# Optimization experiments

Measured on AMD Instinct MI355X. Metric: run time of the kernel, lower is better.

## Reference

```python
import jax, jax.numpy as jnp
import numpy as np

H, W = 14, 14
HEAD_DIM = 32
HEADS = 24
HIDDEN = 768
RATE = 0.2
EPS = 1e-5


def _bias_idxs(h, w):
    # map_bias indexing: for flat pair index x over (h*w)^2
    x = jnp.arange(h * h * w * w)
    m, n = x // (h * w), x % (h * w)
    i, j = m // w, m % w
    ip, jp = n // w, n % w
    return (i - ip + h) * (2 * w) + (j - jp + w)


def _layer_norm(x, g, b):
    mu = jnp.mean(x, axis=-1, keepdims=True)
    var = jnp.mean(jnp.square(x - mu), axis=-1, keepdims=True)
    return (x - mu) * jax.lax.rsqrt(var + EPS) * g + b


def setup_inputs() -> dict:
    key = jax.random.key(0)
    ks = jax.random.split(key, 10)
    N, L = 64, H * W
    s = lambda fan_in: 1.0 / np.sqrt(fan_in)
    return {
        "x": jax.random.normal(ks[0], (N, L, HIDDEN), jnp.float32),
        "rel_bias": jax.random.uniform(ks[1], (1, 2 * H * 2 * W), jnp.float32, -0.5, 0.5),
        "wq": jax.random.normal(ks[2], (HEAD_DIM, HEAD_DIM), jnp.float32) * s(HEAD_DIM),
        "wk": jax.random.normal(ks[3], (HEAD_DIM, HEAD_DIM), jnp.float32) * s(HEAD_DIM),
        "wv": jax.random.normal(ks[4], (HEAD_DIM, HEAD_DIM), jnp.float32) * s(HEAD_DIM),
        "w_out": jax.random.normal(ks[5], (HIDDEN, HIDDEN), jnp.float32) * s(HIDDEN),
        "ln1_g": jnp.ones((HIDDEN,), jnp.float32),
        "ln1_b": jnp.zeros((HIDDEN,), jnp.float32),
        "ln2_g": jnp.ones((HIDDEN,), jnp.float32),
        "ln2_b": jnp.zeros((HIDDEN,), jnp.float32),
        "w1": jax.random.normal(ks[6], (4 * HIDDEN, HIDDEN), jnp.float32) * s(HIDDEN),
        "b1": jnp.zeros((4 * HIDDEN,), jnp.float32),
        "w2": jax.random.normal(ks[7], (HIDDEN, 4 * HIDDEN), jnp.float32) * s(4 * HIDDEN),
        "b2": jnp.zeros((HIDDEN,), jnp.float32),
    }


def reference(x, rel_bias, wq, wk, wv, w_out, ln1_g, ln1_b, ln2_g, ln2_b, w1, b1, w2, b2):
    N, L, _ = x.shape

    def attn(m):
        xh = m.reshape(N, L, HEADS, HEAD_DIM)
        # Linear(head_dim, head_dim) shared across heads; torch Linear: y = x @ W^T
        q = jnp.einsum("nlhd,ed->nlhe", xh, wq)
        k = jnp.einsum("nlhd,ed->nlhe", xh, wk)
        v = jnp.einsum("nlhd,ed->nlhe", xh, wv)
        scores = jnp.einsum("nqhd,nkhd->nhqk", q, k)
        bias = rel_bias[0][_bias_idxs(H, W)].reshape(1, 1, L, L)
        a = jax.nn.softmax((scores + bias) / np.sqrt(HEAD_DIM), axis=-1)
        o = jnp.einsum("nhqk,nkhd->nqhd", a, v).reshape(N, L, HIDDEN)
        return o @ w_out.T

    def ffn(m):
        h = jax.nn.gelu(m @ w1.T + b1, approximate=False)
        return h @ w2.T + b2

    # training-mode stochastic depth: deterministic scaling by RATE
    x = (x + attn(_layer_norm(x, ln1_g, ln1_b))) * RATE
    x = (x + ffn(_layer_norm(x, ln2_g, ln2_b))) * RATE
    return x
```

## Files before the change

### kernel.cpp

```cpp
#include <hip/hip_runtime.h>
#include <math.h>

#define NB    64
#define LSEQ  196
#define HID   768
#define NHEAD 24
#define HDIM  32
#define FFN   3072
#define ROWS  (NB * LSEQ)
#define RATE  0.2f
#define LN_EPS 1e-5f

typedef unsigned short bf16_t;
typedef short s16x8 __attribute__((ext_vector_type(8)));
typedef float f32x4 __attribute__((ext_vector_type(4)));

__device__ __forceinline__ unsigned short f2bf(float f) {
    unsigned u = __float_as_uint(f);
    unsigned r = u + 0x7fffu + ((u >> 16) & 1u);
    return (unsigned short)(r >> 16);
}

#define GLOAD_LDS16(g, l)                                                  \
    __builtin_amdgcn_global_load_lds(                                      \
        (const __attribute__((address_space(1))) void*)(g),                \
        (__attribute__((address_space(3))) void*)(l), 16, 0, 0)

#define WOUT4 (HID * HID / 4)
#define W14   (FFN * HID / 4)
__global__ __launch_bounds__(256) void cvt_w_kernel(
    const float* __restrict__ w_out, const float* __restrict__ w1,
    const float* __restrict__ w2, bf16_t* __restrict__ wob,
    bf16_t* __restrict__ w1b, bf16_t* __restrict__ w2b)
{
    int i = blockIdx.x * 256 + threadIdx.x;
    const float* src; bf16_t* dst; int off;
    if (i < WOUT4)            { src = w_out; dst = wob; off = i; }
    else if (i < WOUT4 + W14) { src = w1;    dst = w1b; off = i - WOUT4; }
    else                      { src = w2;    dst = w2b; off = i - WOUT4 - W14; }
    float4 v = ((const float4*)src)[off];
    uint2 p;
    p.x = (unsigned)f2bf(v.x) | ((unsigned)f2bf(v.y) << 16);
    p.y = (unsigned)f2bf(v.z) | ((unsigned)f2bf(v.w) << 16);
    ((uint2*)dst)[off] = p;
}

__global__ __launch_bounds__(256) void ln_kernel(
    const float* __restrict__ x, const float* __restrict__ g,
    const float* __restrict__ b, bf16_t* __restrict__ yv)
{
    int row = blockIdx.x;
    int tid = threadIdx.x;
    const float* xr = x + (size_t)row * HID;
    float v0 = xr[tid], v1 = xr[tid + 256], v2 = xr[tid + 512];
    __shared__ float rs[256], rs2[256];
    rs[tid]  = v0 + v1 + v2;
    rs2[tid] = v0 * v0 + v1 * v1 + v2 * v2;
    __syncthreads();
    for (int off = 128; off > 0; off >>= 1) {
        if (tid < off) { rs[tid] += rs[tid + off]; rs2[tid] += rs2[tid + off]; }
        __syncthreads();
    }
    float mean = rs[0] * (1.0f / HID);
    float var  = rs2[0] * (1.0f / HID) - mean * mean;
    float rstd = rsqrtf(var + LN_EPS);
    bf16_t* yr = yv + (size_t)row * HID;
    yr[tid]       = f2bf((v0 - mean) * rstd * g[tid]       + b[tid]);
    yr[tid + 256] = f2bf((v1 - mean) * rstd * g[tid + 256] + b[tid + 256]);
    yr[tid + 512] = f2bf((v2 - mean) * rstd * g[tid + 512] + b[tid + 512]);
}

#define QKV_T 16
__global__ __launch_bounds__(256) void ln_qkv_mfma_kernel(
    const float* __restrict__ x, const float* __restrict__ g,
    const float* __restrict__ b,
    const float* __restrict__ wq, const float* __restrict__ wk,
    const float* __restrict__ wv,
    bf16_t* __restrict__ q, bf16_t* __restrict__ k, bf16_t* __restrict__ v)
{
    int tid = threadIdx.x;
    int w = tid >> 6, lane = tid & 63;
    int lr = lane & 15, lq = lane >> 4;

    __shared__ __align__(16) bf16_t Xs[QKV_T * 24 * 32];
    __shared__ __align__(16) bf16_t Wqs[32 * 32];
    __shared__ __align__(16) bf16_t Wks[32 * 32];
    __shared__ __align__(16) bf16_t Wvs[32 * 32];

    for (int i = tid; i < 1024; i += 256) {
        Wqs[i] = f2bf(wq[i]);
        Wks[i] = f2bf(wk[i]);
        Wvs[i] = f2bf(wv[i]);
    }

    float4 gv[3], bv[3];
#pragma unroll
    for (int i = 0; i < 3; i++) {
        gv[i] = ((const float4*)g)[lane + i * 64];
        bv[i] = ((const float4*)b)[lane + i * 64];
    }

    for (int j = 0; j < 4; j++) {
        int lt = w * 4 + j;
        size_t row = (size_t)blockIdx.x * QKV_T + lt;
        const float4* xr = (const float4*)(x + row * HID);
        float4 xv[3];
        float s = 0.f, s2 = 0.f;
#pragma unroll
        for (int i = 0; i < 3; i++) {
            xv[i] = xr[lane + i * 64];
            s  += xv[i].x + xv[i].y + xv[i].z + xv[i].w;
            s2 += xv[i].x * xv[i].x + xv[i].y * xv[i].y
                + xv[i].z * xv[i].z + xv[i].w * xv[i].w;
        }
#pragma unroll
        for (int d = 1; d < 64; d <<= 1) {
            s  += __shfl_xor(s, d);
            s2 += __shfl_xor(s2, d);
        }
        float mean = s * (1.0f / HID);
        float rstd = rsqrtf(s2 * (1.0f / HID) - mean * mean + LN_EPS);
#pragma unroll
        for (int i = 0; i < 3; i++) {
            int idx  = (lane + i * 64) * 4;
            int head = idx >> 5, d0 = idx & 31;
            float o0 = (xv[i].x - mean) * rstd * gv[i].x + bv[i].x;
            float o1 = (xv[i].y - mean) * rstd * gv[i].y + bv[i].y;
            float o2 = (xv[i].z - mean) * rstd * gv[i].z + bv[i].z;
            float o3 = (xv[i].w - mean) * rstd * gv[i].w + bv[i].w;
            uint2 p;
            p.x = (unsigned)f2bf(o0) | ((unsigned)f2bf(o1) << 16);
            p.y = (unsigned)f2bf(o2) | ((unsigned)f2bf(o3) << 16);
            *(uint2*)&Xs[(lt * 24 + head) * 32 + d0] = p;
        }
    }
    __syncthreads();

    s16x8 bq[2], bk[2], bvv[2];
    bq[0]  = *(const s16x8*)&Wqs[lr * 32 + lq * 8];
    bq[1]  = *(const s16x8*)&Wqs[(16 + lr) * 32 + lq * 8];
    bk[0]  = *(const s16x8*)&Wks[lr * 32 + lq * 8];
    bk[1]  = *(const s16x8*)&Wks[(16 + lr) * 32 + lq * 8];
    bvv[0] = *(const s16x8*)&Wvs[lr * 32 + lq * 8];
    bvv[1] = *(const s16x8*)&Wvs[(16 + lr) * 32 + lq * 8];

    for (int t = 0; t < 6; t++) {
        int tile = w * 6 + t;
        s16x8 aX = *(const s16x8*)&Xs[(tile * 16 + lr) * 32 + lq * 8];
        f32x4 z = {};
        f32x4 aq0 = __builtin_amdgcn_mfma_f32_16x16x32_bf16(aX, bq[0],  z, 0, 0, 0);
        f32x4 aq1 = __builtin_amdgcn_mfma_f32_16x16x32_bf16(aX, bq[1],  z, 0, 0, 0);
        f32x4 ak0 = __builtin_amdgcn_mfma_f32_16x16x32_bf16(aX, bk[0],  z, 0, 0, 0);
        f32x4 ak1 = __builtin_amdgcn_mfma_f32_16x16x32_bf16(aX, bk[1],  z, 0, 0, 0);
        f32x4 av0 = __builtin_amdgcn_mfma_f32_16x16x32_bf16(aX, bvv[0], z, 0, 0, 0);
        f32x4 av1 = __builtin_amdgcn_mfma_f32_16x16x32_bf16(aX, bvv[1], z, 0, 0, 0);
        int rbase = tile * 16 + lq * 4;
#pragma unroll
        for (int r = 0; r < 4; r++) {
            int xrow = rbase + r;
            int t_loc = xrow / 24, head = xrow - t_loc * 24;
            size_t gb = ((size_t)blockIdx.x * QKV_T + t_loc) * HID + head * 32;
            q[gb + lr]      = f2bf(aq0[r]);
            q[gb + 16 + lr] = f2bf(aq1[r]);
            k[gb + lr]      = f2bf(ak0[r]);
            k[gb + 16 + lr] = f2bf(ak1[r]);
            v[gb + lr]      = f2bf(av0[r]);
            v[gb + 16 + lr] = f2bf(av1[r]);
        }
    }
}

#define VT_S 232
#define P_S  40

__global__ __launch_bounds__(256) void attn_mfma_kernel(
    const bf16_t* __restrict__ q, const bf16_t* __restrict__ k,
    const bf16_t* __restrict__ v, const float* __restrict__ rel_bias,
    bf16_t* __restrict__ o)
{
    int h = blockIdx.x;
    int n = blockIdx.y;
    int tid = threadIdx.x;
    int w = tid >> 6, lane = tid & 63;
    int lr = lane & 15;
    int lq = lane >> 4;

    __shared__ __align__(16) bf16_t Qs[208 * 32];
    __shared__ __align__(16) bf16_t Ks[224 * 32];
    __shared__ __align__(16) bf16_t Vt[32 * VT_S];
    __shared__ float bsh[28 * 28];
    __shared__ __align__(16) bf16_t Ps[4][16 * P_S];

    size_t base = (size_t)n * LSEQ * HID + (size_t)h * HDIM;

    for (int i = tid; i < 224 * 4; i += 256) {
        int r = i >> 2, c = i & 3;
        uint4 kv = make_uint4(0, 0, 0, 0);
        if (r < 196) kv = *(const uint4*)&k[base + (size_t)r * HID + c * 8];
        *(uint4*)&Ks[r * 32 + c * 8] = kv;
        if (r < 208) {
            uint4 qv = make_uint4(0, 0, 0, 0);
            if (r < 196) qv = *(const uint4*)&q[base + (size_t)r * HID + c * 8];
            *(uint4*)&Qs[r * 32 + c * 8] = qv;
        }
    }
    for (int i = tid; i < 196 * 16; i += 256) {
        int key = i >> 4, d2 = (i & 15) * 2;
        unsigned u = *(const unsigned*)&v[base + (size_t)key * HID + d2];
        Vt[d2 * VT_S + key]       = (bf16_t)(u & 0xffffu);
        Vt[(d2 + 1) * VT_S + key] = (bf16_t)(u >> 16);
    }
    for (int i = tid; i < 32 * 32; i += 256) {
        int d = i >> 5, kp = i & 31;
        if (kp < 28) Vt[d * VT_S + 196 + kp] = 0;
    }
    for (int i = tid; i < 784; i += 256) bsh[i] = rel_bias[i];
    __syncthreads();

    const float inv_sqrt_d = 0.17677669529663687f;
    bf16_t* P = Ps[w];

    for (int qt = w; qt < 13; qt += 4) {
        s16x8 aQ = *(const s16x8*)&Qs[(qt * 16 + lr) * 32 + lq * 8];

        int bb[4]; bool qvalid[4];
#pragma unroll
        for (int r = 0; r < 4; r++) {
            int qr = qt * 16 + lq * 4 + r;
            qvalid[r] = qr < LSEQ;
            int qq = qvalid[r] ? qr : 0;
            int qi = qq / 14, qj = qq - 14 * (qq / 14);
            bb[r] = (qi + 14) * 28 + (qj + 14);
        }

        f32x4 sf[14];
#pragma unroll
        for (int kt = 0; kt < 14; kt++) {
            s16x8 bK = *(const s16x8*)&Ks[(kt * 16 + lr) * 32 + lq * 8];
            f32x4 z = {};
            sf[kt] = __builtin_amdgcn_mfma_f32_16x16x32_bf16(aQ, bK, z, 0, 0, 0);
        }
#pragma unroll
        for (int kt = 0; kt < 14; kt++) {
            int key = kt * 16 + lr;
            bool kv = key < LSEQ;
            int kk2 = kv ? key : 0;
            int ip = kk2 / 14, jp = kk2 - 14 * ip;
            int boff = ip * 28 + jp;
#pragma unroll
            for (int r = 0; r < 4; r++) {
                float val = (sf[kt][r] + bsh[bb[r] - boff]) * inv_sqrt_d;
                sf[kt][r] = kv ? val : -1e30f;
            }
        }
        float mx[4];
#pragma unroll
        for (int r = 0; r < 4; r++) {
            float m = sf[0][r];
#pragma unroll
            for (int kt = 1; kt < 14; kt++) m = fmaxf(m, sf[kt][r]);
            mx[r] = m;
        }
#pragma unroll
        for (int d = 1; d < 16; d <<= 1)
#pragma unroll
            for (int r = 0; r < 4; r++)
                mx[r] = fmaxf(mx[r], __shfl_xor(mx[r], d));
        float sum[4] = {0.f, 0.f, 0.f, 0.f};
#pragma unroll
        for (int kt = 0; kt < 14; kt++)
#pragma unroll
            for (int r = 0; r < 4; r++) {
                float p = __expf(sf[kt][r] - mx[r]);
                sf[kt][r] = p;
                sum[r] += p;
            }
#pragma unroll
        for (int d = 1; d < 16; d <<= 1)
#pragma unroll
            for (int r = 0; r < 4; r++)
                sum[r] += __shfl_xor(sum[r], d);

        f32x4 oacc[2] = {};
#pragma unroll
        for (int kc = 0; kc < 7; kc++) {
#pragma unroll
            for (int r = 0; r < 4; r++) {
                P[(lq * 4 + r) * P_S + lr]      = f2bf(sf[2 * kc][r]);
                P[(lq * 4 + r) * P_S + 16 + lr] = f2bf(sf[2 * kc + 1][r]);
            }
            s16x8 aP = *(const s16x8*)&P[lr * P_S + lq * 8];
#pragma unroll
            for (int dt = 0; dt < 2; dt++) {
                s16x8 bV = *(const s16x8*)&Vt[(dt * 16 + lr) * VT_S + kc * 32 + lq * 8];
                oacc[dt] = __builtin_amdgcn_mfma_f32_16x16x32_bf16(aP, bV, oacc[dt], 0, 0, 0);
            }
        }
#pragma unroll
        for (int r = 0; r < 4; r++) {
            if (qvalid[r]) {
                float inv_l = 1.0f / sum[r];
                size_t ob = base + (size_t)(qt * 16 + lq * 4 + r) * HID;
                o[ob + lr]      = f2bf(oacc[0][r] * inv_l);
                o[ob + 16 + lr] = f2bf(oacc[1][r] * inv_l);
            }
        }
    }
}

__device__ __forceinline__ float gelu_fast(float x) {
    float z2 = 1.5957691216f * (x + 0.044715f * x * x * x);
    return x - x * __frcp_rn(__expf(z2) + 1.0f);
}

template <int MODE, bool OBF, int TM>
__global__ __launch_bounds__(256) void gemm_mfma(
    const bf16_t* __restrict__ A, const bf16_t* __restrict__ B,
    void* __restrict__ Cv, int M, int N, int K,
    const float* __restrict__ bias, const float* __restrict__ res, float scale)
{
    constexpr int MT = TM / 32;
    __shared__ __align__(16) bf16_t As[TM * 64];
    __shared__ __align__(16) bf16_t Bs[128 * 64];

    int tid = threadIdx.x;
    int mb = M / TM, nb = N >> 7;
    int gblk = blockIdx.x;
    int full = mb & ~7;
    int gfull = full * nb;
    int m_, n_;
    if (gblk < gfull) {
        int sg = gblk / (8 * nb), u = gblk - sg * (8 * nb);
        m_ = sg * 8 + (u & 7); n_ = u >> 3;
    } else {
        int u = gblk - gfull, rem = mb - full;
        m_ = full + u % rem; n_ = u / rem;
    }
    int bm = m_ * TM, bn = n_ << 7;

    int w    = tid >> 6;
    int lane = tid & 63;
    int wm = (w & 1) * (TM / 2);
    int wn = (w >> 1) * 64;
    int lr = lane & 15;
    int lq = lane >> 4;

    int srowl = lane >> 3;
    int scb   = ((lane & 7) ^ srowl) * 16;
    const char* Ab = (const char*)A;
    const char* Bb = (const char*)B;

    f32x4 acc[MT][4] = {};

    for (int k0 = 0; k0 < K; k0 += 64) {
#pragma unroll
        for (int j = 0; j < TM / 32; j++) {
            int rb = w * (TM / 4) + j * 8;
            GLOAD_LDS16(Ab + ((size_t)(bm + rb + srowl) * K + k0) * 2 + scb, &As[rb * 64]);
        }
#pragma unroll
        for (int j = 0; j < 4; j++) {
            int rb = w * 32 + j * 8;
            GLOAD_LDS16(Bb + ((size_t)(bn + rb + srowl) * K + k0) * 2 + scb, &Bs[rb * 64]);
        }
        __syncthreads();

        int sw = lr & 7;
#pragma unroll
        for (int kc = 0; kc < 2; kc++) {
            int cof = (((kc << 2) | lq) ^ sw) * 8;
            s16x8 af[MT], bf[4];
#pragma unroll
            for (int t = 0; t < MT; t++)
                af[t] = *(const s16x8*)&As[(wm + t * 16 + lr) * 64 + cof];
#pragma unroll
            for (int t = 0; t < 4; t++)
                bf[t] = *(const s16x8*)&Bs[(wn + t * 16 + lr) * 64 + cof];
#pragma unroll
            for (int tm = 0; tm < MT; tm++)
#pragma unroll
                for (int tn = 0; tn < 4; tn++)
                    acc[tm][tn] = __builtin_amdgcn_mfma_f32_16x16x32_bf16(
                        af[tm], bf[tn], acc[tm][tn], 0, 0, 0);
        }
        __syncthreads();
    }

#pragma unroll
    for (int tm = 0; tm < MT; tm++) {
#pragma unroll
        for (int tn = 0; tn < 4; tn++) {
#pragma unroll
            for (int r = 0; r < 4; r++) {
                int mrow = bm + wm + tm * 16 + lq * 4 + r;
                int ncol = bn + wn + tn * 16 + lr;
                float vacc = acc[tm][tn][r];
                if (MODE == 1) {
                    vacc = (res[(size_t)mrow * N + ncol] + vacc) * scale;
                } else if (MODE == 2) {
                    vacc = gelu_fast(vacc + bias[ncol]);
                } else if (MODE == 3) {
                    vacc = (res[(size_t)mrow * N + ncol] + vacc + bias[ncol]) * scale;
                }
                if (OBF) ((bf16_t*)Cv)[(size_t)mrow * N + ncol] = f2bf(vacc);
                else     ((float*)Cv)[(size_t)mrow * N + ncol] = vacc;
            }
        }
    }
}

template <int MODE, bool OBF>
__global__ __launch_bounds__(512, 2) void gemm_pipe(
    const bf16_t* __restrict__ A, const bf16_t* __restrict__ B,
    void* __restrict__ Cv, int M, int N, int K,
    const float* __restrict__ bias, const float* __restrict__ res, float scale)
{
    constexpr int BM = 256, BN = 128, BK = 64, NBUF = 3;
    __shared__ __align__(16) bf16_t As[NBUF][BM * BK];
    __shared__ __align__(16) bf16_t Bs[NBUF][BN * BK];

    int tid  = threadIdx.x;
    int w    = tid >> 6;
    int lane = tid & 63;

    int mb = M / BM, nb = N / BN;
    int gblk = blockIdx.x;
    int full = mb & ~7;
    int gfull = full * nb;
    int m_, n_;
    if (gblk < gfull) {
        int sg = gblk / (8 * nb), u = gblk - sg * (8 * nb);
        m_ = sg * 8 + (u & 7); n_ = u >> 3;
    } else {
        int u = gblk - gfull, rem = mb - full;
        m_ = full + u % rem; n_ = u / rem;
    }
    int bm = m_ * BM, bn = n_ * BN;

    int wm = (w >> 1) * 64;
    int wn = (w & 1) * 64;
    int lr = lane & 15;
    int lq = lane >> 4;

    int srowl = lane >> 3;
    int scb   = ((lane & 7) ^ srowl) * 16;
    const char* Ab = (const char*)A;
    const char* Bb = (const char*)B;

    const int NT = K / BK;
    f32x4 acc[4][4] = {};

    auto stage = [&](int t, int bi) {
        int k0 = t * BK;
#pragma unroll
        for (int j = 0; j < 4; j++) {
            int rb = j * 64 + w * 8;
            GLOAD_LDS16(Ab + ((size_t)(bm + rb + srowl) * K + k0) * 2 + scb,
                        &As[bi][rb * BK]);
        }
#pragma unroll
        for (int j = 0; j < 2; j++) {
            int rb = j * 64 + w * 8;
            GLOAD_LDS16(Bb + ((size_t)(bn + rb + srowl) * K + k0) * 2 + scb,
                        &Bs[bi][rb * BK]);
        }
    };

    auto compute = [&](int bi) {
        int sw = lr & 7;
        __builtin_amdgcn_s_setprio(1);
#pragma unroll
        for (int kc = 0; kc < 2; kc++) {
            int cof = (((kc << 2) | lq) ^ sw) * 8;
            s16x8 af[4], bf[4];
#pragma unroll
            for (int t = 0; t < 4; t++)
                af[t] = *(const s16x8*)&As[bi][(wm + t * 16 + lr) * BK + cof];
#pragma unroll
            for (int t = 0; t < 4; t++)
                bf[t] = *(const s16x8*)&Bs[bi][(wn + t * 16 + lr) * BK + cof];
#pragma unroll
            for (int tm = 0; tm < 4; tm++)
#pragma unroll
                for (int tn = 0; tn < 4; tn++)
                    acc[tm][tn] = __builtin_amdgcn_mfma_f32_16x16x32_bf16(
                        af[tm], bf[tn], acc[tm][tn], 0, 0, 0);
        }
        __builtin_amdgcn_s_setprio(0);
    };

    stage(0, 0);
    stage(1, 1);

    for (int t = 0; t < NT - 2; t++) {
        stage(t + 2, (t + 2) % 3);
        asm volatile("s_waitcnt vmcnt(12)" ::: "memory");
        __builtin_amdgcn_s_barrier();
        asm volatile("" ::: "memory");
        compute(t % 3);
        asm volatile("" ::: "memory");
        __builtin_amdgcn_s_barrier();
    }
    asm volatile("s_waitcnt vmcnt(6)" ::: "memory");
    __builtin_amdgcn_s_barrier();
    asm volatile("" ::: "memory");
    compute((NT - 2) % 3);
    asm volatile("s_waitcnt vmcnt(0)" ::: "memory");
    __builtin_amdgcn_s_barrier();
    asm volatile("" ::: "memory");
    compute((NT - 1) % 3);

#pragma unroll
    for (int tm = 0; tm < 4; tm++) {
#pragma unroll
        for (int tn = 0; tn < 4; tn++) {
#pragma unroll
            for (int r = 0; r < 4; r++) {
                int mrow = bm + wm + tm * 16 + lq * 4 + r;
                int ncol = bn + wn + tn * 16 + lr;
                float vacc = acc[tm][tn][r];
                if (MODE == 1) {
                    vacc = (res[(size_t)mrow * N + ncol] + vacc) * scale;
                } else if (MODE == 2) {
                    vacc = gelu_fast(vacc + bias[ncol]);
                } else if (MODE == 3) {
                    vacc = (res[(size_t)mrow * N + ncol] + vacc + bias[ncol]) * scale;
                }
                if (OBF) ((bf16_t*)Cv)[(size_t)mrow * N + ncol] = f2bf(vacc);
                else     ((float*)Cv)[(size_t)mrow * N + ncol] = vacc;
            }
        }
    }
}

extern "C" void kernel_launch(void* const* d_in, const int* in_sizes, int n_in,
                              void* d_out, int out_size, void* d_ws, size_t ws_size,
                              hipStream_t stream)
{
    const float* x        = (const float*)d_in[0];
    const float* rel_bias = (const float*)d_in[1];
    const float* wq       = (const float*)d_in[2];
    const float* wk       = (const float*)d_in[3];
    const float* wv       = (const float*)d_in[4];
    const float* w_out    = (const float*)d_in[5];
    const float* ln1_g    = (const float*)d_in[6];
    const float* ln1_b    = (const float*)d_in[7];
    const float* ln2_g    = (const float*)d_in[8];
    const float* ln2_b    = (const float*)d_in[9];
    const float* w1       = (const float*)d_in[10];
    const float* b1       = (const float*)d_in[11];
    const float* w2       = (const float*)d_in[12];
    const float* b2       = (const float*)d_in[13];
    float* out = (float*)d_out;
    float* ws  = (float*)d_ws;

    const size_t SZ = (size_t)ROWS * HID;
    bf16_t* q_bf = (bf16_t*)(ws + SZ);
    bf16_t* k_bf = (bf16_t*)(ws + 2 * SZ);
    bf16_t* v_bf = (bf16_t*)(ws + 3 * SZ);
    bf16_t* o_bf = (bf16_t*)ws;
    bf16_t* y2b  = (bf16_t*)(ws + SZ / 2);
    bf16_t* h    = (bf16_t*)(ws + SZ);
    bf16_t* wob  = (bf16_t*)(ws + 4 * SZ);
    bf16_t* w1b  = wob + (size_t)HID * HID;
    bf16_t* w2b  = w1b + (size_t)FFN * HID;

    cvt_w_kernel<<<(WOUT4 + 2 * W14 + 255) / 256, 256, 0, stream>>>(
        w_out, w1, w2, wob, w1b, w2b);

    ln_qkv_mfma_kernel<<<ROWS / QKV_T, 256, 0, stream>>>(
        x, ln1_g, ln1_b, wq, wk, wv, q_bf, k_bf, v_bf);

    attn_mfma_kernel<<<dim3(NHEAD, NB), 256, 0, stream>>>(q_bf, k_bf, v_bf, rel_bias, o_bf);

    gemm_mfma<1, false, 64><<<(ROWS / 64) * (HID / 128), 256, 0, stream>>>(
        o_bf, wob, out, ROWS, HID, HID, nullptr, x, RATE);

    ln_kernel<<<ROWS, 256, 0, stream>>>(out, ln2_g, ln2_b, y2b);

    gemm_pipe<2, true><<<(ROWS / 256) * (FFN / 128), 512, 0, stream>>>(
        y2b, w1b, h, ROWS, FFN, HID, b1, nullptr, 1.0f);

    gemm_pipe<3, false><<<(ROWS / 256) * (HID / 128), 512, 0, stream>>>(
        h, w2b, out, ROWS, HID, FFN, b2, out, RATE);
}
```

Before: 499.1 us.

## Double-buffer small GEMM and swap FFN GEMMs to wide/single-buffered tiles

Result: faster. 483.4 us (-3.1%).

```diff
diff --git a/kernel.cpp b/kernel.cpp
--- a/kernel.cpp
+++ b/kernel.cpp
@@ -320,8 +320,8 @@
     const float* __restrict__ bias, const float* __restrict__ res, float scale)
 {
     constexpr int MT = TM / 32;
-    __shared__ __align__(16) bf16_t As[TM * 64];
-    __shared__ __align__(16) bf16_t Bs[128 * 64];
+    __shared__ __align__(16) bf16_t As[2][TM * 64];
+    __shared__ __align__(16) bf16_t Bs[2][128 * 64];
 
     int tid = threadIdx.x;
     int mb = M / TM, nb = N >> 7;
@@ -352,19 +352,22 @@
 
     f32x4 acc[MT][4] = {};
 
-    for (int k0 = 0; k0 < K; k0 += 64) {
+    auto stage = [&](int k0, int bi) {
 #pragma unroll
         for (int j = 0; j < TM / 32; j++) {
             int rb = w * (TM / 4) + j * 8;
-            GLOAD_LDS16(Ab + ((size_t)(bm + rb + srowl) * K + k0) * 2 + scb, &As[rb * 64]);
+            GLOAD_LDS16(Ab + ((size_t)(bm + rb + srowl) * K + k0) * 2 + scb,
+                        &As[bi][rb * 64]);
         }
 #pragma unroll
         for (int j = 0; j < 4; j++) {
             int rb = w * 32 + j * 8;
-            GLOAD_LDS16(Bb + ((size_t)(bn + rb + srowl) * K + k0) * 2 + scb, &Bs[rb * 64]);
-        }
-        __syncthreads();
-
+            GLOAD_LDS16(Bb + ((size_t)(bn + rb + srowl) * K + k0) * 2 + scb,
+                        &Bs[bi][rb * 64]);
+        }
+    };
+
+    auto compute = [&](int bi) {
         int sw = lr & 7;
 #pragma unroll
         for (int kc = 0; kc < 2; kc++) {
@@ -372,10 +375,10 @@
             s16x8 af[MT], bf[4];
 #pragma unroll
             for (int t = 0; t < MT; t++)
-                af[t] = *(const s16x8*)&As[(wm + t * 16 + lr) * 64 + cof];
+                af[t] = *(const s16x8*)&As[bi][(wm + t * 16 + lr) * 64 + cof];
 #pragma unroll
             for (int t = 0; t < 4; t++)
-                bf[t] = *(const s16x8*)&Bs[(wn + t * 16 + lr) * 64 + cof];
+                bf[t] = *(const s16x8*)&Bs[bi][(wn + t * 16 + lr) * 64 + cof];
 #pragma unroll
             for (int tm = 0; tm < MT; tm++)
 #pragma unroll
@@ -383,8 +386,22 @@
                     acc[tm][tn] = __builtin_amdgcn_mfma_f32_16x16x32_bf16(
                         af[tm], bf[tn], acc[tm][tn], 0, 0, 0);
         }
-        __syncthreads();
-    }
+    };
+
+    stage(0, 0);
+    asm volatile("s_waitcnt vmcnt(0)" ::: "memory");
+    __builtin_amdgcn_s_barrier();
+
+    const int nt = K >> 6;
+    int cur = 0;
+    for (int t = 0; t < nt - 1; ++t) {
+        stage((t + 1) << 6, cur ^ 1);
+        compute(cur);
+        asm volatile("s_waitcnt vmcnt(0)" ::: "memory");
+        __builtin_amdgcn_s_barrier();
+        cur ^= 1;
+    }
+    compute(cur);
 
 #pragma unroll
     for (int tm = 0; tm < MT; tm++) {
@@ -410,20 +427,16 @@
 }
 
 template <int MODE, bool OBF>
-__global__ __launch_bounds__(512, 2) void gemm_pipe(
+__global__ __launch_bounds__(256) void gemm_wide(
     const bf16_t* __restrict__ A, const bf16_t* __restrict__ B,
     void* __restrict__ Cv, int M, int N, int K,
     const float* __restrict__ bias, const float* __restrict__ res, float scale)
 {
-    constexpr int BM = 256, BN = 128, BK = 64, NBUF = 3;
-    __shared__ __align__(16) bf16_t As[NBUF][BM * BK];
-    __shared__ __align__(16) bf16_t Bs[NBUF][BN * BK];
-
-    int tid  = threadIdx.x;
-    int w    = tid >> 6;
-    int lane = tid & 63;
-
-    int mb = M / BM, nb = N / BN;
+    __shared__ __align__(16) bf16_t As[128 * 64];
+    __shared__ __align__(16) bf16_t Bs[256 * 64];
+
+    int tid = threadIdx.x;
+    int mb = M >> 7, nb = N >> 8;
     int gblk = blockIdx.x;
     int full = mb & ~7;
     int gfull = full * nb;
@@ -435,10 +448,11 @@
         int u = gblk - gfull, rem = mb - full;
         m_ = full + u % rem; n_ = u / rem;
     }
-    int bm = m_ * BM, bn = n_ * BN;
-
-    int wm = (w >> 1) * 64;
-    int wn = (w & 1) * 64;
+    int bm = m_ << 7, bn = n_ << 8;
+
+    int w    = tid >> 6;
+    int lane = tid & 63;
+    int wn = w * 64;
     int lr = lane & 15;
     int lq = lane >> 4;
 
@@ -447,76 +461,51 @@
     const char* Ab = (const char*)A;
     const char* Bb = (const char*)B;
 
-    const int NT = K / BK;
-    f32x4 acc[4][4] = {};
-
-    auto stage = [&](int t, int bi) {
-        int k0 = t * BK;
+    f32x4 acc[8][4] = {};
+
+    for (int k0 = 0; k0 < K; k0 += 64) {
 #pragma unroll
         for (int j = 0; j < 4; j++) {
-            int rb = j * 64 + w * 8;
+            int rb = j * 32 + w * 8;
             GLOAD_LDS16(Ab + ((size_t)(bm + rb + srowl) * K + k0) * 2 + scb,
-                        &As[bi][rb * BK]);
-        }
-#pragma unroll
-        for (int j = 0; j < 2; j++) {
-            int rb = j * 64 + w * 8;
+                        &As[rb * 64]);
+        }
+#pragma unroll
+        for (int j = 0; j < 8; j++) {
+            int rb = j * 32 + w * 8;
             GLOAD_LDS16(Bb + ((size_t)(bn + rb + srowl) * K + k0) * 2 + scb,
-                        &Bs[bi][rb * BK]);
-        }
-    };
-
-    auto compute = [&](int bi) {
+                        &Bs[rb * 64]);
+        }
+        __syncthreads();
+
         int sw = lr & 7;
-        __builtin_amdgcn_s_setprio(1);
 #pragma unroll
         for (int kc = 0; kc < 2; kc++) {
             int cof = (((kc << 2) | lq) ^ sw) * 8;
-            s16x8 af[4], bf[4];
+            s16x8 af[8], bf[4];
+#pragma unroll
+            for (int t = 0; t < 8; t++)
+                af[t] = *(const s16x8*)&As[(t * 16 + lr) * 64 + cof];
 #pragma unroll
             for (int t = 0; t < 4; t++)
-                af[t] = *(const s16x8*)&As[bi][(wm + t * 16 + lr) * BK + cof];
-#pragma unroll
-            for (int t = 0; t < 4; t++)
-                bf[t] = *(const s16x8*)&Bs[bi][(wn + t * 16 + lr) * BK + cof];
-#pragma unroll
-            for (int tm = 0; tm < 4; tm++)
+                bf[t] = *(const s16x8*)&Bs[(wn + t * 16 + lr) * 64 + cof];
+#pragma unroll
+            for (int tm = 0; tm < 8; tm++)
 #pragma unroll
                 for (int tn = 0; tn < 4; tn++)
                     acc[tm][tn] = __builtin_amdgcn_mfma_f32_16x16x32_bf16(
                         af[tm], bf[tn], acc[tm][tn], 0, 0, 0);
         }
-        __builtin_amdgcn_s_setprio(0);
-    };
-
-    stage(0, 0);
-    stage(1, 1);
-
-    for (int t = 0; t < NT - 2; t++) {
-        stage(t + 2, (t + 2) % 3);
-        asm volatile("s_waitcnt vmcnt(12)" ::: "memory");
-        __builtin_amdgcn_s_barrier();
-        asm volatile("" ::: "memory");
-        compute(t % 3);
-        asm volatile("" ::: "memory");
-        __builtin_amdgcn_s_barrier();
-    }
-    asm volatile("s_waitcnt vmcnt(6)" ::: "memory");
-    __builtin_amdgcn_s_barrier();
-    asm volatile("" ::: "memory");
-    compute((NT - 2) % 3);
-    asm volatile("s_waitcnt vmcnt(0)" ::: "memory");
-    __builtin_amdgcn_s_barrier();
-    asm volatile("" ::: "memory");
-    compute((NT - 1) % 3);
-
-#pragma unroll
-    for (int tm = 0; tm < 4; tm++) {
+        __syncthreads();
+    }
+
+#pragma unroll
+    for (int tm = 0; tm < 8; tm++) {
 #pragma unroll
         for (int tn = 0; tn < 4; tn++) {
 #pragma unroll
             for (int r = 0; r < 4; r++) {
-                int mrow = bm + wm + tm * 16 + lq * 4 + r;
+                int mrow = bm + tm * 16 + lq * 4 + r;
                 int ncol = bn + wn + tn * 16 + lr;
                 float vacc = acc[tm][tn][r];
                 if (MODE == 1) {
@@ -578,9 +567,9 @@
 
     ln_kernel<<<ROWS, 256, 0, stream>>>(out, ln2_g, ln2_b, y2b);
 
-    gemm_pipe<2, true><<<(ROWS / 256) * (FFN / 128), 512, 0, stream>>>(
+    gemm_wide<2, true><<<(ROWS / 128) * (FFN / 256), 256, 0, stream>>>(
         y2b, w1b, h, ROWS, FFN, HID, b1, nullptr, 1.0f);
 
-    gemm_pipe<3, false><<<(ROWS / 256) * (HID / 128), 512, 0, stream>>>(
+    gemm_mfma<3, false, 64><<<(ROWS / 64) * (HID / 128), 256, 0, stream>>>(
         h, w2b, out, ROWS, HID, FFN, b2, out, RATE);
 }
```

## Double-buffer small GEMM, split FFN1 pipeline into phases, route FFN2 to small GEMM

Applied to the files above, without the earlier changes.

Measured after the change: 433.8 us. -13.1%, faster.

```diff
diff --git a/kernel.cpp b/kernel.cpp
--- a/kernel.cpp
+++ b/kernel.cpp
@@ -320,8 +320,8 @@
     const float* __restrict__ bias, const float* __restrict__ res, float scale)
 {
     constexpr int MT = TM / 32;
-    __shared__ __align__(16) bf16_t As[TM * 64];
-    __shared__ __align__(16) bf16_t Bs[128 * 64];
+    __shared__ __align__(16) bf16_t As[2][TM * 64];
+    __shared__ __align__(16) bf16_t Bs[2][128 * 64];
 
     int tid = threadIdx.x;
     int mb = M / TM, nb = N >> 7;
@@ -352,19 +352,22 @@
 
     f32x4 acc[MT][4] = {};
 
-    for (int k0 = 0; k0 < K; k0 += 64) {
+    auto stage = [&](int k0, int bi) {
 #pragma unroll
         for (int j = 0; j < TM / 32; j++) {
             int rb = w * (TM / 4) + j * 8;
-            GLOAD_LDS16(Ab + ((size_t)(bm + rb + srowl) * K + k0) * 2 + scb, &As[rb * 64]);
+            GLOAD_LDS16(Ab + ((size_t)(bm + rb + srowl) * K + k0) * 2 + scb,
+                        &As[bi][rb * 64]);
         }
 #pragma unroll
         for (int j = 0; j < 4; j++) {
             int rb = w * 32 + j * 8;
-            GLOAD_LDS16(Bb + ((size_t)(bn + rb + srowl) * K + k0) * 2 + scb, &Bs[rb * 64]);
-        }
-        __syncthreads();
-
+            GLOAD_LDS16(Bb + ((size_t)(bn + rb + srowl) * K + k0) * 2 + scb,
+                        &Bs[bi][rb * 64]);
+        }
+    };
+
+    auto compute = [&](int bi) {
         int sw = lr & 7;
 #pragma unroll
         for (int kc = 0; kc < 2; kc++) {
@@ -372,10 +375,10 @@
             s16x8 af[MT], bf[4];
 #pragma unroll
             for (int t = 0; t < MT; t++)
-                af[t] = *(const s16x8*)&As[(wm + t * 16 + lr) * 64 + cof];
+                af[t] = *(const s16x8*)&As[bi][(wm + t * 16 + lr) * 64 + cof];
 #pragma unroll
             for (int t = 0; t < 4; t++)
-                bf[t] = *(const s16x8*)&Bs[(wn + t * 16 + lr) * 64 + cof];
+                bf[t] = *(const s16x8*)&Bs[bi][(wn + t * 16 + lr) * 64 + cof];
 #pragma unroll
             for (int tm = 0; tm < MT; tm++)
 #pragma unroll
@@ -383,8 +386,22 @@
                     acc[tm][tn] = __builtin_amdgcn_mfma_f32_16x16x32_bf16(
                         af[tm], bf[tn], acc[tm][tn], 0, 0, 0);
         }
-        __syncthreads();
-    }
+    };
+
+    stage(0, 0);
+    asm volatile("s_waitcnt vmcnt(0)" ::: "memory");
+    __builtin_amdgcn_s_barrier();
+
+    const int nt = K >> 6;
+    int cur = 0;
+    for (int t = 0; t < nt - 1; ++t) {
+        stage((t + 1) << 6, cur ^ 1);
+        compute(cur);
+        asm volatile("s_waitcnt vmcnt(0)" ::: "memory");
+        __builtin_amdgcn_s_barrier();
+        cur ^= 1;
+    }
+    compute(cur);
 
 #pragma unroll
     for (int tm = 0; tm < MT; tm++) {
@@ -410,7 +427,7 @@
 }
 
 template <int MODE, bool OBF>
-__global__ __launch_bounds__(512, 2) void gemm_pipe(
+__global__ __launch_bounds__(512, 2) void gemm_fph(
     const bf16_t* __restrict__ A, const bf16_t* __restrict__ B,
     void* __restrict__ Cv, int M, int N, int K,
     const float* __restrict__ bias, const float* __restrict__ res, float scale)
@@ -447,68 +464,85 @@
     const char* Ab = (const char*)A;
     const char* Bb = (const char*)B;
 
+    f32x4 acc[4][4] = {};
+
+    auto stageA = [&](int t, int bi, int j) {
+        int rb = j * 64 + w * 8;
+        GLOAD_LDS16(Ab + ((size_t)(bm + rb + srowl) * K + t * BK) * 2 + scb,
+                    &As[bi][rb * BK]);
+    };
+    auto stageB = [&](int t, int bi, int j) {
+        int rb = j * 64 + w * 8;
+        GLOAD_LDS16(Bb + ((size_t)(bn + rb + srowl) * K + t * BK) * 2 + scb,
+                    &Bs[bi][rb * BK]);
+    };
+
     const int NT = K / BK;
-    f32x4 acc[4][4] = {};
-
-    auto stage = [&](int t, int bi) {
-        int k0 = t * BK;
-#pragma unroll
-        for (int j = 0; j < 4; j++) {
-            int rb = j * 64 + w * 8;
-            GLOAD_LDS16(Ab + ((size_t)(bm + rb + srowl) * K + k0) * 2 + scb,
-                        &As[bi][rb * BK]);
-        }
-#pragma unroll
-        for (int j = 0; j < 2; j++) {
-            int rb = j * 64 + w * 8;
-            GLOAD_LDS16(Bb + ((size_t)(bn + rb + srowl) * K + k0) * 2 + scb,
-                        &Bs[bi][rb * BK]);
-        }
-    };
-
-    auto compute = [&](int bi) {
-        int sw = lr & 7;
-        __builtin_amdgcn_s_setprio(1);
-#pragma unroll
-        for (int kc = 0; kc < 2; kc++) {
-            int cof = (((kc << 2) | lq) ^ sw) * 8;
-            s16x8 af[4], bf[4];
-#pragma unroll
-            for (int t = 0; t < 4; t++)
-                af[t] = *(const s16x8*)&As[bi][(wm + t * 16 + lr) * BK + cof];
-#pragma unroll
-            for (int t = 0; t < 4; t++)
-                bf[t] = *(const s16x8*)&Bs[bi][(wn + t * 16 + lr) * BK + cof];
+    int sw = lr & 7;
+
+    stageA(0, 0, 0); stageA(0, 0, 1); stageA(0, 0, 2); stageA(0, 0, 3);
+    stageB(0, 0, 0); stageB(0, 0, 1);
+    stageA(1, 1, 0); stageA(1, 1, 1); stageA(1, 1, 2); stageA(1, 1, 3);
+    stageB(1, 1, 0); stageB(1, 1, 1);
+    asm volatile("s_waitcnt vmcnt(6)" ::: "memory");
+    __builtin_amdgcn_s_barrier();
+
+    for (int t = 0; t < NT; ++t) {
+        int ct = t % 3;
+        bool st = (t + 2) < NT;
+        int bs2 = (t + 2) % 3;
+        const bf16_t* Ac = As[ct];
+        const bf16_t* Bc = Bs[ct];
+
+        {
+            int cof = ((lq) ^ sw) * 8;
+            s16x8 af[4], bf4[4];
+#pragma unroll
+            for (int i = 0; i < 4; i++)
+                af[i] = *(const s16x8*)&Ac[(wm + i * 16 + lr) * BK + cof];
+#pragma unroll
+            for (int i = 0; i < 4; i++)
+                bf4[i] = *(const s16x8*)&Bc[(wn + i * 16 + lr) * BK + cof];
+            if (st) { stageA(t + 2, bs2, 0); stageA(t + 2, bs2, 1); stageA(t + 2, bs2, 2); }
+            __builtin_amdgcn_s_barrier();
+            __builtin_amdgcn_s_setprio(1);
 #pragma unroll
             for (int tm = 0; tm < 4; tm++)
 #pragma unroll
                 for (int tn = 0; tn < 4; tn++)
                     acc[tm][tn] = __builtin_amdgcn_mfma_f32_16x16x32_bf16(
-                        af[tm], bf[tn], acc[tm][tn], 0, 0, 0);
-        }
-        __builtin_amdgcn_s_setprio(0);
-    };
-
-    stage(0, 0);
-    stage(1, 1);
-
-    for (int t = 0; t < NT - 2; t++) {
-        stage(t + 2, (t + 2) % 3);
-        asm volatile("s_waitcnt vmcnt(12)" ::: "memory");
+                        af[tm], bf4[tn], acc[tm][tn], 0, 0, 0);
+            __builtin_amdgcn_s_setprio(0);
+        }
         __builtin_amdgcn_s_barrier();
-        asm volatile("" ::: "memory");
-        compute(t % 3);
-        asm volatile("" ::: "memory");
-        __builtin_amdgcn_s_barrier();
-    }
-    asm volatile("s_waitcnt vmcnt(6)" ::: "memory");
-    __builtin_amdgcn_s_barrier();
-    asm volatile("" ::: "memory");
-    compute((NT - 2) % 3);
-    asm volatile("s_waitcnt vmcnt(0)" ::: "memory");
-    __builtin_amdgcn_s_barrier();
-    asm volatile("" ::: "memory");
-    compute((NT - 1) % 3);
+
+        {
+            int cof = ((4 | lq) ^ sw) * 8;
+            s16x8 af[4], bf4[4];
+#pragma unroll
+            for (int i = 0; i < 4; i++)
+                af[i] = *(const s16x8*)&Ac[(wm + i * 16 + lr) * BK + cof];
+#pragma unroll
+            for (int i = 0; i < 4; i++)
+                bf4[i] = *(const s16x8*)&Bc[(wn + i * 16 + lr) * BK + cof];
+            if (st) { stageA(t + 2, bs2, 3); stageB(t + 2, bs2, 0); stageB(t + 2, bs2, 1); }
+            __builtin_amdgcn_s_barrier();
+            __builtin_amdgcn_s_setprio(1);
+#pragma unroll
+            for (int tm = 0; tm < 4; tm++)
+#pragma unroll
+                for (int tn = 0; tn < 4; tn++)
+                    acc[tm][tn] = __builtin_amdgcn_mfma_f32_16x16x32_bf16(
+                        af[tm], bf4[tn], acc[tm][tn], 0, 0, 0);
+            __builtin_amdgcn_s_setprio(0);
+        }
+
+        if (t < NT - 1) {
+            if (st) asm volatile("s_waitcnt vmcnt(6)" ::: "memory");
+            else    asm volatile("s_waitcnt vmcnt(0)" ::: "memory");
+            __builtin_amdgcn_s_barrier();
+        }
+    }
 
 #pragma unroll
     for (int tm = 0; tm < 4; tm++) {
@@ -578,9 +612,9 @@
 
     ln_kernel<<<ROWS, 256, 0, stream>>>(out, ln2_g, ln2_b, y2b);
 
-    gemm_pipe<2, true><<<(ROWS / 256) * (FFN / 128), 512, 0, stream>>>(
+    gemm_fph<2, true><<<(ROWS / 256) * (FFN / 128), 512, 0, stream>>>(
         y2b, w1b, h, ROWS, FFN, HID, b1, nullptr, 1.0f);
 
-    gemm_pipe<3, false><<<(ROWS / 256) * (HID / 128), 512, 0, stream>>>(
+    gemm_mfma<3, false, 64><<<(ROWS / 64) * (HID / 128), 256, 0, stream>>>(
         h, w2b, out, ROWS, HID, FFN, b2, out, RATE);
 }
```
